# Kernel optimization log

Measured on AMD Instinct MI355X. Metric: run time of the kernel, lower is better.

Reference implementation:

```python
import jax, jax.numpy as jnp
import numpy as np

B = 256
NUM_PRIMARY = 32      # cfg.num_primary_caps
PRIM_ATOMS = 8
NUM_CLASSES = 10
DIGIT_ATOMS = 16
NUM_ROUTING = 3       # cfg.num_routing (DigitCap)
IN_DIM = 6 * 6 * NUM_PRIMARY  # 1152
NUM_PIXELS = 28 * 28 * 1


def squash(s, axis):
    # v = ||s||^2/(1+||s||^2) * s/||s||
    n2 = jnp.sum(jnp.square(s), axis=axis, keepdims=True)
    return s * (n2 / (1.0 + n2)) / jnp.sqrt(n2 + 1e-9)


def conv2d(x, w, stride):
    return jax.lax.conv_general_dilated(
        x, w, (stride, stride), 'VALID',
        dimension_numbers=('NCHW', 'OIHW', 'NCHW'))


def setup_inputs() -> dict:
    key = jax.random.key(0)
    ks = jax.random.split(key, 10)
    x = jax.random.uniform(ks[0], (B, 1, 28, 28), jnp.float32)
    labels = jax.random.randint(ks[1], (B,), 0, NUM_CLASSES)
    y = jax.nn.one_hot(labels, NUM_CLASSES, dtype=jnp.float32)
    conv1_w = 0.05 * jax.random.normal(ks[2], (256, 1, 9, 9), jnp.float32)
    conv1_b = jnp.full((256,), 0.1, jnp.float32)
    # primary capsule conv: 256 -> 32 caps * 8 atoms, k=9, s=2 (bias applied after routing)
    prim_w = 0.05 * jax.random.normal(ks[3], (NUM_PRIMARY * PRIM_ATOMS, 256, 9, 9), jnp.float32)
    prim_b = jnp.full((NUM_PRIMARY, PRIM_ATOMS), 0.1, jnp.float32)
    # digit capsule transform: [in_dim, in_atoms, out_dim, out_atoms]
    digit_w = 0.05 * jax.random.normal(ks[4], (IN_DIM, PRIM_ATOMS, NUM_CLASSES, DIGIT_ATOMS), jnp.float32)
    digit_b = jnp.full((NUM_CLASSES, DIGIT_ATOMS), 0.1, jnp.float32)
    w1 = 0.05 * jax.random.normal(ks[5], (NUM_CLASSES * DIGIT_ATOMS, 512), jnp.float32)
    b1 = jnp.zeros((512,), jnp.float32)
    w2 = 0.05 * jax.random.normal(ks[6], (512, 1024), jnp.float32)
    b2 = jnp.zeros((1024,), jnp.float32)
    w3 = 0.05 * jax.random.normal(ks[7], (1024, NUM_PIXELS), jnp.float32)
    b3 = jnp.zeros((NUM_PIXELS,), jnp.float32)
    return dict(x=x, y=y, conv1_w=conv1_w, conv1_b=conv1_b, prim_w=prim_w,
                prim_b=prim_b, digit_w=digit_w, digit_b=digit_b,
                w1=w1, b1=b1, w2=w2, b2=b2, w3=w3, b3=b3)


def reference(x, y, conv1_w, conv1_b, prim_w, prim_b, digit_w, digit_b,
              w1, b1, w2, b2, w3, b3):
    # conv stem
    h = jax.nn.relu(conv2d(x, conv1_w, 1) + conv1_b[None, :, None, None])  # [B,256,20,20]

    # PrimaryCap: conv votes [B, in_dim=1, out=32, atoms=8, 6, 6]; num_routing=1
    votes_p = conv2d(h, prim_w, 2).reshape(B, NUM_PRIMARY, PRIM_ATOMS, 6, 6)
    # one routing iter, input_dim=1: softmax(zeros) over output_dim -> uniform 1/32
    preact_p = votes_p / NUM_PRIMARY + prim_b[None, :, :, None, None]
    caps1 = squash(preact_p, axis=2)  # [B,32,8,6,6]

    # permute(0,1,3,4,2) then flatten -> [B, 1152, 8]
    x3 = jnp.transpose(caps1, (0, 1, 3, 4, 2)).reshape(B, IN_DIM, PRIM_ATOMS)

    # DigitCap votes: [B, in_dim, out_dim, out_atoms]
    votes = jnp.einsum('bia,iaot->biot', x3, digit_w)
    logits = jnp.zeros((B, IN_DIM, NUM_CLASSES), votes.dtype)
    act = None
    for _ in range(NUM_ROUTING):
        route = jax.nn.softmax(logits, axis=2)  # over output capsules
        preact = jnp.einsum('bio,biot->bot', route, votes) + digit_b
        act = squash(preact, axis=-1)  # [B,10,16]
        logits = logits + jnp.einsum('biot,bot->bio', votes, act)
    digit = act

    # Reconstruction: mask by label, 160 -> 512 -> 1024 -> 784
    masked = (digit * y[:, :, None]).reshape(B, NUM_CLASSES * DIGIT_ATOMS)
    r = jax.nn.relu(masked @ w1 + b1)
    r = jax.nn.relu(r @ w2 + b2)
    recon = jax.nn.sigmoid(r @ w3 + b3)
    return digit, recon
```

## Files before the change

### kernel.cpp

```cpp
#include <hip/hip_runtime.h>
#include <hip/hip_bf16.h>

typedef unsigned short u16;
typedef unsigned int u32;

static __device__ __forceinline__ float us2f(u16 u) {
    return __uint_as_float(((u32)u) << 16);
}
static __device__ __forceinline__ u16 f2bu(float f) {
    u32 u = __float_as_uint(f);
    return (u16)((u + 0x7fffu + ((u >> 16) & 1u)) >> 16);
}

typedef __attribute__((ext_vector_type(8))) __bf16 bf16x8;
typedef __attribute__((ext_vector_type(4))) float f32x4;

static __device__ __forceinline__ void async16(const u16* g, u16* l) {
    __builtin_amdgcn_global_load_lds(
        (const __attribute__((address_space(1))) unsigned int*)g,
        (__attribute__((address_space(3))) unsigned int*)l, 16, 0, 0);
}

__global__ void fill_sentinel(float* out, int n, float val) {
    int g = blockIdx.x * 256 + threadIdx.x;
    if (g < n) out[g] = val;
}

__global__ __launch_bounds__(256) void prep1(const float* __restrict__ pw,
    u16* __restrict__ wt, float* __restrict__ x3m,
    const float* __restrict__ c1w, u16* __restrict__ wc1b)
{
    __shared__ u16 wl[81 * 258];
    const int bid = blockIdx.x, tid = threadIdx.x;
    if (bid < 256) {
        const float* ws = pw + (size_t)bid * 20736;
        for (int idx = tid; idx < 20736; idx += 256) {
            const int cc = idx / 81, kk = idx - cc * 81;
            wl[kk * 258 + cc] = f2bu(ws[idx]);
        }
        __syncthreads();
        u16* wo = wt + (size_t)bid * 20736;
        for (int q = tid; q < 20736; q += 256)
            wo[q] = wl[(q >> 8) * 258 + (q & 255)];
    } else if (bid < 2548) {
        float4 z = {0.f, 0.f, 0.f, 0.f};
        reinterpret_cast<float4*>(x3m)[(size_t)(bid - 256) * 256 + tid] = z;
    } else {
        for (int idx = tid; idx < 24576; idx += 256) {
            const int s = idx >> 13, rem = idx & 8191;
            const int n = rem >> 5, kk = rem & 31;
            const int k = s * 32 + kk;
            wc1b[idx] = (k < 81) ? f2bu(c1w[n * 81 + k]) : (u16)0;
        }
    }
}

__global__ __launch_bounds__(256) void prep2(const float* __restrict__ dw,
    u16* __restrict__ dwb_t, float* __restrict__ preactD)
{
    const int bid = blockIdx.x, tid = threadIdx.x;
    if (bid < 5760) {
        const int g = bid * 256 + tid;
        dwb_t[g] = f2bu(dw[g]);
    } else {
        float4 z = {0.f, 0.f, 0.f, 0.f};
        reinterpret_cast<float4*>(preactD)[(size_t)(bid - 5760) * 256 + tid] = z;
    }
}

__global__ __launch_bounds__(256, 2) void conv1_mfma(const float* __restrict__ x,
    const u16* __restrict__ wc1b, const float* __restrict__ bias, u16* __restrict__ h)
{
    __shared__ float xs[1568];
    const int tid = threadIdx.x;
    const int mBase = blockIdx.x * 128;
    const int b0 = mBase / 400;
    const int lane = tid & 63, wv = tid >> 6;
    const int wm = wv >> 1, wn = wv & 1;
    const int lcol = lane & 15, lquad = lane >> 4;

    {
        const int b1 = (b0 + 1 < 256) ? b0 + 1 : b0;
        for (int i = tid; i < 784; i += 256) {
            xs[i] = x[b0 * 784 + i];
            xs[784 + i] = x[b1 * 784 + i];
        }
    }
    __syncthreads();

    float bj[8];
    #pragma unroll
    for (int j = 0; j < 8; ++j) bj[j] = bias[wn * 128 + j * 16 + lcol];

    int xbase[4];
    #pragma unroll
    for (int i = 0; i < 4; ++i) {
        const int m = mBase + wm * 64 + i * 16 + lcol;
        const int img = (m / 400) - b0;
        const int rr = m % 400;
        const int iy = rr / 20, ix = rr - iy * 20;
        xbase[i] = img * 784 + iy * 28 + ix;
    }

    f32x4 acc[4][8];
    #pragma unroll
    for (int i = 0; i < 4; ++i)
        #pragma unroll
        for (int j = 0; j < 8; ++j) acc[i][j] = (f32x4){0.f, 0.f, 0.f, 0.f};

    #pragma unroll 1
    for (int s = 0; s < 3; ++s) {
        bf16x8 bfr[8];
        const u16* bp = wc1b + s * 8192 + (wn * 128 + lcol) * 32 + lquad * 8;
        #pragma unroll
        for (int j = 0; j < 8; ++j)
            bfr[j] = *reinterpret_cast<const bf16x8*>(bp + j * 512);

        bf16x8 ah[4], al[4];
        #pragma unroll
        for (int i = 0; i < 4; ++i) {
            union { bf16x8 v; u16 u[8]; } H, L;
            #pragma unroll
            for (int e = 0; e < 8; ++e) {
                int k = s * 32 + lquad * 8 + e;
                if (k > 80) k = 0;
                const int dy = k / 9, dx = k - dy * 9;
                const float xv = xs[xbase[i] + dy * 28 + dx];
                const u16 hu = f2bu(xv);
                H.u[e] = hu;
                L.u[e] = f2bu(xv - us2f(hu));
            }
            ah[i] = H.v; al[i] = L.v;
        }
        #pragma unroll
        for (int i = 0; i < 4; ++i)
            #pragma unroll
            for (int j = 0; j < 8; ++j) {
                acc[i][j] = __builtin_amdgcn_mfma_f32_16x16x32_bf16(ah[i], bfr[j], acc[i][j], 0, 0, 0);
                acc[i][j] = __builtin_amdgcn_mfma_f32_16x16x32_bf16(al[i], bfr[j], acc[i][j], 0, 0, 0);
            }
    }

    #pragma unroll
    for (int i = 0; i < 4; ++i) {
        const int mrow = mBase + wm * 64 + i * 16 + lquad * 4;
        #pragma unroll
        for (int j = 0; j < 8; ++j) {
            const int ncol = wn * 128 + j * 16 + lcol;
            #pragma unroll
            for (int r = 0; r < 4; ++r)
                h[(size_t)(mrow + r) * 256 + ncol] = f2bu(fmaxf(acc[i][j][r] + bj[j], 0.f));
        }
    }
}

__global__ __launch_bounds__(256, 2) void prim_gemm_split(const u16* __restrict__ h,
    const u16* __restrict__ wT, float* __restrict__ pm)
{
    __shared__ u16 As[3 * 4096];
    __shared__ u16 Bs[3 * 8192];
    const int tid = threadIdx.x;
    const int split = blockIdx.y;
    const int mBase = blockIdx.x * 128;
    const int lane = tid & 63, wv = tid >> 6;
    const int swzq = (tid & 3) ^ ((lane >> 3) & 3);
    const int rA = wv * 32 + (lane >> 2);
    const int rB = wv * 64 + (lane >> 2);
    int mA0 = mBase + rA;
    int bA0 = mA0 / 36, rr0 = mA0 % 36;
    const int aBase0 = ((bA0 * 20 + 2 * (rr0 / 6)) * 20 + 2 * (rr0 % 6)) * 256 + swzq * 8;
    int mA1 = mA0 + 16;
    int bA1 = mA1 / 36, rr1 = mA1 % 36;
    const int aBase1 = ((bA1 * 20 + 2 * (rr1 / 6)) * 20 + 2 * (rr1 % 6)) * 256 + swzq * 8;
    const u16* bp0 = wT + (size_t)rB * 20736 + swzq * 8;

    int kglob = split * 3456;
    int ky = kglob / 2304; int krem = kglob - ky * 2304;
    int kx = krem >> 8; int c0 = krem & 255;

    f32x4 acc[4][8];
    #pragma unroll
    for (int i = 0; i < 4; ++i)
        #pragma unroll
        for (int j = 0; j < 8; ++j) acc[i][j] = (f32x4){0.f, 0.f, 0.f, 0.f};

    const int wm = wv >> 1, wn = wv & 1;
    const int lcol = lane & 15, lquad = lane >> 4;
    const int rswz = (lquad ^ ((lcol >> 1) & 3)) * 8;
    const u16* Arow = As + (wm * 64 + lcol) * 32 + rswz;
    const u16* Brow = Bs + (wn * 128 + lcol) * 32 + rswz;
    u16* aD = As + wv * 1024;
    u16* bD = Bs + wv * 2048;

    #define STAGE(sel)  do {                                                   \
        const int koffA = (ky * 20 + kx) * 256 + c0;                           \
        async16(h + aBase0 + koffA, aD + (sel) * 4096);                        \
        async16(h + aBase1 + koffA, aD + (sel) * 4096 + 512);                  \
        async16(bp0 + kglob,          bD + (sel) * 8192);                      \
        async16(bp0 + 331776 + kglob, bD + (sel) * 8192 + 512);               \
        async16(bp0 + 663552 + kglob, bD + (sel) * 8192 + 1024);              \
        async16(bp0 + 995328 + kglob, bD + (sel) * 8192 + 1536);              \
        kglob += 32; c0 += 32;                                                 \
        if (c0 == 256) { c0 = 0; if (++kx == 9) { kx = 0; ++ky; } }            \
    } while (0)

    #define COMPUTE(sel)  do {                                                 \
        const u16* Ab = Arow + (sel) * 4096;                                   \
        const u16* Bb = Brow + (sel) * 8192;                                   \
        bf16x8 af[4], bfr[8];                                                  \
        _Pragma("unroll")                                                      \
        for (int i = 0; i < 4; ++i)                                            \
            af[i] = *reinterpret_cast<const bf16x8*>(Ab + i * 512);            \
        _Pragma("unroll")                                                      \
        for (int j = 0; j < 8; ++j)                                            \
            bfr[j] = *reinterpret_cast<const bf16x8*>(Bb + j * 512);           \
        __builtin_amdgcn_s_setprio(1);                                         \
        _Pragma("unroll")                                                      \
        for (int i = 0; i < 4; ++i)                                            \
            _Pragma("unroll")                                                  \
            for (int j = 0; j < 8; ++j)                                        \
                acc[i][j] = __builtin_amdgcn_mfma_f32_16x16x32_bf16(af[i], bfr[j], acc[i][j], 0, 0, 0); \
        __builtin_amdgcn_s_setprio(0);                                         \
    } while (0)

    STAGE(0);
    STAGE(1);
    int cb = 0, sb = 2;
    #pragma unroll 1
    for (int kt = 0; kt < 106; ++kt) {
        STAGE(sb);
        asm volatile("s_waitcnt vmcnt(12)" ::: "memory");
        __builtin_amdgcn_s_barrier();
        __builtin_amdgcn_sched_barrier(0);
        COMPUTE(cb);
        __builtin_amdgcn_sched_barrier(0);
        __builtin_amdgcn_s_barrier();
        __builtin_amdgcn_sched_barrier(0);
        cb = (cb == 2) ? 0 : cb + 1;
        sb = (sb == 2) ? 0 : sb + 1;
    }
    asm volatile("s_waitcnt vmcnt(6)" ::: "memory");
    __builtin_amdgcn_s_barrier();
    __builtin_amdgcn_sched_barrier(0);
    COMPUTE(1);
    __builtin_amdgcn_sched_barrier(0);
    asm volatile("s_waitcnt vmcnt(0)" ::: "memory");
    __builtin_amdgcn_s_barrier();
    __builtin_amdgcn_sched_barrier(0);
    COMPUTE(2);
    #undef STAGE
    #undef COMPUTE

    #pragma unroll
    for (int i = 0; i < 4; ++i) {
        const int mrow = mBase + wm * 64 + i * 16 + lquad * 4;
        #pragma unroll
        for (int j = 0; j < 8; ++j) {
            const int ncol = wn * 128 + j * 16 + lcol;
            #pragma unroll
            for (int r = 0; r < 4; ++r)
                unsafeAtomicAdd(&pm[(size_t)(mrow + r) * 256 + ncol], acc[i][j][r]);
        }
    }
}

__global__ __launch_bounds__(192) void votes_gemm(const float* __restrict__ x3m,
    const float* __restrict__ pb, const u16* __restrict__ dwb_t,
    u16* __restrict__ votes, int hb)
{
    __shared__ float dws[8 * 1280];
    __shared__ float x3s[64 * 64];
    __shared__ float pbs[256];
    const int ic = blockIdx.x * 8, bc = blockIdx.y * 64;
    const int tid = threadIdx.x;
    for (int q = tid; q < 256; q += 192) pbs[q] = pb[q];
    for (int q = tid; q < 10240; q += 192)
        dws[q] = us2f(dwb_t[(size_t)ic * 1280 + q]);
    __syncthreads();
    for (int g = tid; g < 512; g += 192) {
        const int b_l = g >> 3, i_l = g & 7;
        const int i = ic + i_l, cap = i / 36, p = i - cap * 36;
        const float* src = &x3m[((size_t)(hb + bc + b_l) * 36 + p) * 256 + cap * 8];
        float v[8]; float n2 = 0.f;
        #pragma unroll
        for (int a = 0; a < 8; ++a) {
            v[a] = src[a] * (1.f / 32.f) + pbs[cap * 8 + a];
            n2 += v[a] * v[a];
        }
        const float scale = (n2 / (1.f + n2)) * rsqrtf(n2 + 1e-9f);
        #pragma unroll
        for (int a = 0; a < 8; ++a)
            x3s[b_l * 64 + i_l * 8 + a] = v[a] * scale;
    }
    __syncthreads();
    if (tid < 160) {
        const int ot = tid;
        float dwr[8][8];
        #pragma unroll
        for (int i_l = 0; i_l < 8; ++i_l)
            #pragma unroll
            for (int a = 0; a < 8; ++a)
                dwr[i_l][a] = dws[i_l * 1280 + a * 160 + ot];
        #pragma unroll 1
        for (int b_l = 0; b_l < 64; ++b_l) {
            u16 ob[8];
            #pragma unroll
            for (int i_l = 0; i_l < 8; ++i_l) {
                const float* xp = &x3s[b_l * 64 + i_l * 8];
                float v = 0.f;
                #pragma unroll
                for (int a = 0; a < 8; ++a) v += xp[a] * dwr[i_l][a];
                ob[i_l] = f2bu(v);
            }
            uint4 o4;
            o4.x = (u32)ob[0] | ((u32)ob[1] << 16);
            o4.y = (u32)ob[2] | ((u32)ob[3] << 16);
            o4.z = (u32)ob[4] | ((u32)ob[5] << 16);
            o4.w = (u32)ob[6] | ((u32)ob[7] << 16);
            *reinterpret_cast<uint4*>(&votes[((size_t)(bc + b_l) * 160 + ot) * 1152 + ic]) = o4;
        }
    }
}

__global__ __launch_bounds__(256) void routing_fused(const u16* __restrict__ votes,
    const float* __restrict__ pD_prev, const float* __restrict__ db,
    float* __restrict__ logits, float* __restrict__ pD_next, int hb, int mode)
{
    __shared__ u16 vs16[160 * 146];
    __shared__ float route_s[144 * 10];
    __shared__ float act_s[160];
    const int ic = blockIdx.x * 144, b_l = blockIdx.y, gb = hb + b_l;
    const int tid = threadIdx.x;

    for (int q = tid; q < 2880; q += 256) {
        const int ot = q / 18, ch = q - ot * 18;
        const uint4 d = *reinterpret_cast<const uint4*>(
            &votes[((size_t)b_l * 160 + ot) * 1152 + ic + ch * 8]);
        u32* vp = reinterpret_cast<u32*>(&vs16[ot * 146 + ch * 8]);
        vp[0] = d.x; vp[1] = d.y; vp[2] = d.z; vp[3] = d.w;
    }
    if (mode >= 1 && tid < 160) {
        float pre = pD_prev[(size_t)gb * 160 + tid] + db[tid];
        float sq = pre * pre;
        sq += __shfl_xor(sq, 1); sq += __shfl_xor(sq, 2);
        sq += __shfl_xor(sq, 4); sq += __shfl_xor(sq, 8);
        act_s[tid] = pre * (sq / (1.f + sq)) * rsqrtf(sq + 1e-9f);
    }
    __syncthreads();

    if (mode >= 1) {
        if (tid < 144) {
            float acc[10];
            #pragma unroll
            for (int k = 0; k < 10; ++k) acc[k] = 0.f;
            #pragma unroll 4
            for (int ot = 0; ot < 160; ++ot)
                acc[ot >> 4] += us2f(vs16[ot * 146 + tid]) * act_s[ot];
            float* lp = &logits[((size_t)gb * 1152 + ic + tid) * 10];
            float l[10];
            if (mode == 1) {
                #pragma unroll
                for (int k = 0; k < 10; ++k) { l[k] = acc[k]; lp[k] = l[k]; }
            } else {
                #pragma unroll
                for (int k = 0; k < 10; ++k) { l[k] = lp[k] + acc[k]; lp[k] = l[k]; }
            }
            float mx = -1e30f;
            #pragma unroll
            for (int k = 0; k < 10; ++k) mx = fmaxf(mx, l[k]);
            float s = 0.f;
            #pragma unroll
            for (int k = 0; k < 10; ++k) { l[k] = __expf(l[k] - mx); s += l[k]; }
            const float inv = 1.f / s;
            #pragma unroll
            for (int k = 0; k < 10; ++k) route_s[tid * 10 + k] = l[k] * inv;
        }
        __syncthreads();
    }

    if (tid < 160) {
        const int o = tid >> 4;
        const u16* vrow = &vs16[tid * 146];
        float acc2 = 0.f;
        if (mode == 0) {
            float s = 0.f;
            #pragma unroll 8
            for (int i = 0; i < 144; ++i) s += us2f(vrow[i]);
            acc2 = 0.1f * s;
        } else {
            const float* rp = &route_s[o];
            #pragma unroll 8
            for (int i = 0; i < 144; ++i)
                acc2 += rp[i * 10] * us2f(vrow[i]);
        }
        unsafeAtomicAdd(&pD_next[(size_t)gb * 160 + tid], acc2);
    }
}

__global__ __launch_bounds__(256) void mlp_layer(const float* __restrict__ in,
    const float* __restrict__ maskY, const float* __restrict__ w,
    const float* __restrict__ bias, float* __restrict__ outp, int K, int N, int mode,
    const float* __restrict__ db2, float* __restrict__ dout)
{
    __shared__ float ins[4 * 1024];
    __shared__ float scl[40];
    const int b0 = blockIdx.x * 4;
    const int n = blockIdx.y * 256 + threadIdx.x;
    if (db2) {
        if (threadIdx.x < 40) {
            const int b_l = threadIdx.x / 10, o = threadIdx.x - b_l * 10;
            const float* pp = &in[(size_t)(b0 + b_l) * 160 + o * 16];
            float n2 = 0.f;
            #pragma unroll
            for (int t = 0; t < 16; ++t) {
                float pv = pp[t] + db2[o * 16 + t];
                n2 += pv * pv;
            }
            scl[threadIdx.x] = (n2 / (1.f + n2)) * rsqrtf(n2 + 1e-9f);
        }
        __syncthreads();
        for (int idx = threadIdx.x; idx < 4 * 160; idx += 256) {
            const int b_l = idx / 160, j = idx - b_l * 160;
            float a = (in[(size_t)(b0 + b_l) * 160 + j] + db2[j]) * scl[b_l * 10 + (j >> 4)];
            if (blockIdx.y == 0 && dout) dout[(size_t)(b0 + b_l) * 160 + j] = a;
            ins[idx] = a * maskY[(b0 + b_l) * 10 + (j >> 4)];
        }
    } else {
        for (int idx = threadIdx.x; idx < 4 * K; idx += 256) {
            float v = in[(size_t)b0 * K + idx];
            if (maskY) {
                const int b_l = idx / K, j = idx % K;
                v *= maskY[(b0 + b_l) * 10 + (j >> 4)];
            }
            ins[idx] = v;
        }
    }
    __syncthreads();
    if (n < N) {
        float a0 = 0.f, a1 = 0.f, a2 = 0.f, a3 = 0.f;
        for (int k = 0; k < K; ++k) {
            const float wvv = w[(size_t)k * N + n];
            a0 += ins[k] * wvv;
            a1 += ins[K + k] * wvv;
            a2 += ins[2 * K + k] * wvv;
            a3 += ins[3 * K + k] * wvv;
        }
        const float bv = bias[n];
        float v[4] = {a0 + bv, a1 + bv, a2 + bv, a3 + bv};
        #pragma unroll
        for (int j = 0; j < 4; ++j) {
            float xv = v[j];
            xv = (mode == 0) ? fmaxf(xv, 0.f) : 1.f / (1.f + __expf(-xv));
            outp[(size_t)(b0 + j) * N + n] = xv;
        }
    }
}

extern "C" void kernel_launch(void* const* d_in, const int* in_sizes, int n_in,
                              void* d_out, int out_size, void* d_ws, size_t ws_size,
                              hipStream_t stream) {
    const float* x   = (const float*)d_in[0];
    const float* y   = (const float*)d_in[1];
    const float* c1w = (const float*)d_in[2];
    const float* c1b = (const float*)d_in[3];
    const float* pw  = (const float*)d_in[4];
    const float* pb  = (const float*)d_in[5];
    const float* dw  = (const float*)d_in[6];
    const float* db  = (const float*)d_in[7];
    const float* w1  = (const float*)d_in[8];
    const float* b1  = (const float*)d_in[9];
    const float* w2  = (const float*)d_in[10];
    const float* b2  = (const float*)d_in[11];
    const float* w3  = (const float*)d_in[12];
    const float* b3  = (const float*)d_in[13];
    float* out = (float*)d_out;
    char* ws = (char*)d_ws;

    static const int exp_sizes[14] = {200704, 2560, 20736, 256, 5308416, 256,
                                      1474560, 160, 81920, 512, 524288, 1024,
                                      802816, 784};
    int bad = (n_in == 14) ? -1 : -2;
    if (bad == -1)
        for (int i = 0; i < 14; ++i) if (in_sizes[i] != exp_sizes[i]) { bad = i; break; }
    if (bad != -1) {
        fill_sentinel<<<(out_size + 255) / 256, 256, 0, stream>>>(out, out_size,
            7168.f + 16.f * (float)(bad + 1));
        return;
    }
    const size_t NEEDED = 72482816ULL;
    if (ws_size < NEEDED) {
        fill_sentinel<<<(out_size + 255) / 256, 256, 0, stream>>>(out, out_size, 111.0f);
        return;
    }

    u16*   h       = (u16*)(ws);
    u16*   wT2     = (u16*)(ws + 52428800);
    float* x3m     = (float*)(ws + 63045632);
    u16*   wc1b    = (u16*)(ws + 72433664);
    u16*   votes   = (u16*)(ws);
    float* logits  = (float*)(ws + 47185920);
    float* preactD = (float*)(ws + 59146240);
    u16*   dwb_t   = (u16*)(ws + 59637760);
    float* r1      = (float*)(ws + 62586880);
    float* r2      = (float*)(ws + 63111168);

    prep1<<<2549, 256, 0, stream>>>(pw, wT2, x3m, c1w, wc1b);
    conv1_mfma<<<800, 256, 0, stream>>>(x, wc1b, c1b, h);
    hipMemsetAsync(wc1b, 0, 49152, stream);
    prim_gemm_split<<<dim3(72, 6), 256, 0, stream>>>(h, wT2, x3m);
    prep2<<<5880, 256, 0, stream>>>(dw, dwb_t, preactD);

    float* pD0 = preactD, *pD1 = preactD + 40960, *pD2 = preactD + 81920;
    for (int half = 0; half < 2; ++half) {
        const int hb = half * 128;
        votes_gemm<<<dim3(144, 2), 192, 0, stream>>>(x3m, pb, dwb_t, votes, hb);
        routing_fused<<<dim3(8, 128), 256, 0, stream>>>(votes, pD0, db, logits, pD0, hb, 0);
        routing_fused<<<dim3(8, 128), 256, 0, stream>>>(votes, pD0, db, logits, pD1, hb, 1);
        routing_fused<<<dim3(8, 128), 256, 0, stream>>>(votes, pD1, db, logits, pD2, hb, 2);
    }

    mlp_layer<<<dim3(64, 2), 256, 0, stream>>>(pD2, y, w1, b1, r1, 160, 512, 0, db, out);
    mlp_layer<<<dim3(64, 4), 256, 0, stream>>>(r1, (float*)nullptr, w2, b2, r2, 512, 1024, 0,
                                               (const float*)nullptr, (float*)nullptr);
    mlp_layer<<<dim3(64, 4), 256, 0, stream>>>(r2, (float*)nullptr, w3, b3, out + 40960, 1024, 784, 1,
                                               (const float*)nullptr, (float*)nullptr);
}
```

Baseline: 720.1 us.

## Fuse three routing iterations into one per-sample kernel with logits in LDS

Replaces the three routing_fused launches, each a grid of 8 input-chunk blocks per sample, with a single routing_all kernel that runs one 512-thread block per sample. Each block streams its sample's votes through double-buffered LDS chunks three times. Logits stay in shared memory and partial preactivations accumulate in registers, so the global logits buffer and the atomics are gone. The cost is much less parallelism: only 128 blocks per half, far fewer than the 1024 blocks per launch before, on a GPU with many CUs. The votes are also re-read from global memory on every pass.

```diff
diff --git a/kernel.cpp b/kernel.cpp
--- a/kernel.cpp
+++ b/kernel.cpp
@@ -322,79 +322,167 @@
     }
 }
 
-__global__ __launch_bounds__(256) void routing_fused(const u16* __restrict__ votes,
-    const float* __restrict__ pD_prev, const float* __restrict__ db,
-    float* __restrict__ logits, float* __restrict__ pD_next, int hb, int mode)
+__global__ __launch_bounds__(512, 1) void routing_all(const u16* __restrict__ votes,
+    const float* __restrict__ db, float* __restrict__ pD2, int hb)
 {
-    __shared__ u16 vs16[160 * 146];
-    __shared__ float route_s[144 * 10];
+    __shared__ u16 vch[2][160 * 130];
+    __shared__ float lg[11520];
+    __shared__ float route_s[1280];
     __shared__ float act_s[160];
-    const int ic = blockIdx.x * 144, b_l = blockIdx.y, gb = hb + b_l;
+    const int b_l = blockIdx.x, gb = hb + b_l;
     const int tid = threadIdx.x;
-
-    for (int q = tid; q < 2880; q += 256) {
-        const int ot = q / 18, ch = q - ot * 18;
-        const uint4 d = *reinterpret_cast<const uint4*>(
-            &votes[((size_t)b_l * 160 + ot) * 1152 + ic + ch * 8]);
-        u32* vp = reinterpret_cast<u32*>(&vs16[ot * 146 + ch * 8]);
-        vp[0] = d.x; vp[1] = d.y; vp[2] = d.z; vp[3] = d.w;
-    }
-    if (mode >= 1 && tid < 160) {
-        float pre = pD_prev[(size_t)gb * 160 + tid] + db[tid];
-        float sq = pre * pre;
-        sq += __shfl_xor(sq, 1); sq += __shfl_xor(sq, 2);
-        sq += __shfl_xor(sq, 4); sq += __shfl_xor(sq, 8);
-        act_s[tid] = pre * (sq / (1.f + sq)) * rsqrtf(sq + 1e-9f);
-    }
-    __syncthreads();
-
-    if (mode >= 1) {
-        if (tid < 144) {
-            float acc[10];
-            #pragma unroll
-            for (int k = 0; k < 10; ++k) acc[k] = 0.f;
-            #pragma unroll 4
-            for (int ot = 0; ot < 160; ++ot)
-                acc[ot >> 4] += us2f(vs16[ot * 146 + tid]) * act_s[ot];
-            float* lp = &logits[((size_t)gb * 1152 + ic + tid) * 10];
-            float l[10];
-            if (mode == 1) {
-                #pragma unroll
-                for (int k = 0; k < 10; ++k) { l[k] = acc[k]; lp[k] = l[k]; }
-            } else {
-                #pragma unroll
-                for (int k = 0; k < 10; ++k) { l[k] = lp[k] + acc[k]; lp[k] = l[k]; }
-            }
-            float mx = -1e30f;
-            #pragma unroll
-            for (int k = 0; k < 10; ++k) mx = fmaxf(mx, l[k]);
-            float s = 0.f;
-            #pragma unroll
-            for (int k = 0; k < 10; ++k) { l[k] = __expf(l[k] - mx); s += l[k]; }
-            const float inv = 1.f / s;
-            #pragma unroll
-            for (int k = 0; k < 10; ++k) route_s[tid * 10 + k] = l[k] * inv;
-        }
-        __syncthreads();
-    }
-
-    if (tid < 160) {
-        const int o = tid >> 4;
-        const u16* vrow = &vs16[tid * 146];
-        float acc2 = 0.f;
-        if (mode == 0) {
+    const u16* vb = votes + (size_t)b_l * 184320;
+    const int iq = tid >> 2, gq = tid & 3;
+    const float dbv = (tid < 160) ? db[tid] : 0.f;
+    uint4 pf[5];
+
+#define LOADC(c) do {                                                          \
+    _Pragma("unroll")                                                          \
+    for (int r = 0; r < 5; ++r) {                                              \
+        const int q = tid + r * 512;                                           \
+        pf[r] = *reinterpret_cast<const uint4*>(                               \
+            vb + (q >> 4) * 1152 + (c) * 128 + (q & 15) * 8);                  \
+    } } while (0)
+
+#define WRITEC(buf) do {                                                       \
+    _Pragma("unroll")                                                          \
+    for (int r = 0; r < 5; ++r) {                                              \
+        const int q = tid + r * 512;                                           \
+        u32* d = reinterpret_cast<u32*>(&vch[buf][(q >> 4) * 130 + (q & 15) * 8]); \
+        d[0] = pf[r].x; d[1] = pf[r].y; d[2] = pf[r].z; d[3] = pf[r].w;        \
+    } } while (0)
+
+#define SQUASH_TO_ACT(preexpr) do {                                            \
+    if (tid < 160) {                                                           \
+        float pre = (preexpr) + dbv;                                           \
+        float sq = pre * pre;                                                  \
+        sq += __shfl_xor(sq, 1); sq += __shfl_xor(sq, 2);                      \
+        sq += __shfl_xor(sq, 4); sq += __shfl_xor(sq, 8);                      \
+        act_s[tid] = pre * (sq / (1.f + sq)) * rsqrtf(sq + 1e-9f);             \
+    }                                                                          \
+    __syncthreads();                                                           \
+} while (0)
+
+    float accP = 0.f;
+    LOADC(0); WRITEC(0); __syncthreads();
+    #pragma unroll 1
+    for (int c = 0; c < 9; ++c) {
+        if (c < 8) LOADC(c + 1);
+        if (tid < 160) {
+            const u16* vrow = &vch[c & 1][tid * 130];
             float s = 0.f;
             #pragma unroll 8
-            for (int i = 0; i < 144; ++i) s += us2f(vrow[i]);
-            acc2 = 0.1f * s;
-        } else {
-            const float* rp = &route_s[o];
+            for (int i = 0; i < 128; ++i) s += us2f(vrow[i]);
+            accP += s;
+        }
+        if (c < 8) WRITEC((c + 1) & 1);
+        __syncthreads();
+    }
+    SQUASH_TO_ACT(0.1f * accP);
+
+    float pP = 0.f;
+    LOADC(0); WRITEC(0); __syncthreads();
+    #pragma unroll 1
+    for (int c = 0; c < 9; ++c) {
+        if (c < 8) LOADC(c + 1);
+        {
+            const u16* vcol = &vch[c & 1][gq * 5200 + iq];
+            float u[10];
+            #pragma unroll
+            for (int k = 0; k < 10; ++k) u[k] = 0.f;
             #pragma unroll 8
-            for (int i = 0; i < 144; ++i)
-                acc2 += rp[i * 10] * us2f(vrow[i]);
-        }
-        unsafeAtomicAdd(&pD_next[(size_t)gb * 160 + tid], acc2);
-    }
+            for (int t = 0; t < 40; ++t) {
+                const int ot = gq * 40 + t;
+                u[ot >> 4] += us2f(vcol[t * 130]) * act_s[ot];
+            }
+            #pragma unroll
+            for (int k = 0; k < 10; ++k) {
+                u[k] += __shfl_xor(u[k], 1);
+                u[k] += __shfl_xor(u[k], 2);
+            }
+            const int gi = c * 128 + iq;
+            if (gq == 0) {
+                #pragma unroll
+                for (int k = 0; k < 10; ++k) lg[gi * 10 + k] = u[k];
+            }
+            float mx = -1e30f;
+            #pragma unroll
+            for (int k = 0; k < 10; ++k) mx = fmaxf(mx, u[k]);
+            float s = 0.f;
+            #pragma unroll
+            for (int k = 0; k < 10; ++k) { u[k] = __expf(u[k] - mx); s += u[k]; }
+            const float inv = 1.f / s;
+            if (gq == 0) {
+                #pragma unroll
+                for (int k = 0; k < 10; ++k) route_s[iq * 10 + k] = u[k] * inv;
+            }
+        }
+        __syncthreads();
+        if (tid < 160) {
+            const int o = tid >> 4;
+            const u16* vrow = &vch[c & 1][tid * 130];
+            float s = 0.f;
+            #pragma unroll 8
+            for (int i = 0; i < 128; ++i) s += route_s[i * 10 + o] * us2f(vrow[i]);
+            pP += s;
+        }
+        if (c < 8) WRITEC((c + 1) & 1);
+        __syncthreads();
+    }
+    SQUASH_TO_ACT(pP);
+
+    float pP2 = 0.f;
+    LOADC(0); WRITEC(0); __syncthreads();
+    #pragma unroll 1
+    for (int c = 0; c < 9; ++c) {
+        if (c < 8) LOADC(c + 1);
+        {
+            const u16* vcol = &vch[c & 1][gq * 5200 + iq];
+            float u[10];
+            #pragma unroll
+            for (int k = 0; k < 10; ++k) u[k] = 0.f;
+            #pragma unroll 8
+            for (int t = 0; t < 40; ++t) {
+                const int ot = gq * 40 + t;
+                u[ot >> 4] += us2f(vcol[t * 130]) * act_s[ot];
+            }
+            #pragma unroll
+            for (int k = 0; k < 10; ++k) {
+                u[k] += __shfl_xor(u[k], 1);
+                u[k] += __shfl_xor(u[k], 2);
+            }
+            const int gi = c * 128 + iq;
+            #pragma unroll
+            for (int k = 0; k < 10; ++k) u[k] += lg[gi * 10 + k];
+            float mx = -1e30f;
+            #pragma unroll
+            for (int k = 0; k < 10; ++k) mx = fmaxf(mx, u[k]);
+            float s = 0.f;
+            #pragma unroll
+            for (int k = 0; k < 10; ++k) { u[k] = __expf(u[k] - mx); s += u[k]; }
+            const float inv = 1.f / s;
+            if (gq == 0) {
+                #pragma unroll
+                for (int k = 0; k < 10; ++k) route_s[iq * 10 + k] = u[k] * inv;
+            }
+        }
+        __syncthreads();
+        if (tid < 160) {
+            const int o = tid >> 4;
+            const u16* vrow = &vch[c & 1][tid * 130];
+            float s = 0.f;
+            #pragma unroll 8
+            for (int i = 0; i < 128; ++i) s += route_s[i * 10 + o] * us2f(vrow[i]);
+            pP2 += s;
+        }
+        if (c < 8) WRITEC((c + 1) & 1);
+        __syncthreads();
+    }
+    if (tid < 160)
+        pD2[(size_t)gb * 160 + tid] = pP2;
+#undef LOADC
+#undef WRITEC
+#undef SQUASH_TO_ACT
 }
 
 __global__ __launch_bounds__(256) void mlp_layer(const float* __restrict__ in,
@@ -498,7 +586,6 @@
     float* x3m     = (float*)(ws + 63045632);
     u16*   wc1b    = (u16*)(ws + 72433664);
     u16*   votes   = (u16*)(ws);
-    float* logits  = (float*)(ws + 47185920);
     float* preactD = (float*)(ws + 59146240);
     u16*   dwb_t   = (u16*)(ws + 59637760);
     float* r1      = (float*)(ws + 62586880);
@@ -510,13 +597,11 @@
     prim_gemm_split<<<dim3(72, 6), 256, 0, stream>>>(h, wT2, x3m);
     prep2<<<5880, 256, 0, stream>>>(dw, dwb_t, preactD);
 
-    float* pD0 = preactD, *pD1 = preactD + 40960, *pD2 = preactD + 81920;
+    float* pD2 = preactD + 81920;
     for (int half = 0; half < 2; ++half) {
         const int hb = half * 128;
         votes_gemm<<<dim3(144, 2), 192, 0, stream>>>(x3m, pb, dwb_t, votes, hb);
-        routing_fused<<<dim3(8, 128), 256, 0, stream>>>(votes, pD0, db, logits, pD0, hb, 0);
-        routing_fused<<<dim3(8, 128), 256, 0, stream>>>(votes, pD0, db, logits, pD1, hb, 1);
-        routing_fused<<<dim3(8, 128), 256, 0, stream>>>(votes, pD1, db, logits, pD2, hb, 2);
+        routing_all<<<128, 512, 0, stream>>>(votes, db, pD2, hb);
     }
 
     mlp_layer<<<dim3(64, 2), 256, 0, stream>>>(pD2, y, w1, b1, r1, 160, 512, 0, db, out);
```

New measurement: 875.4 us. 1.22x slower.
